# Performance work log

Measured on AMD Instinct MI355X. Metric: run time of the kernel, lower is better.

## Reference

```python
import jax, jax.numpy as jnp
import numpy as np

B, T_ENC, T_DEC = 32, 300, 500
N_MEL, ENC_DIM, ATT_RNN, DEC_RNN, PRE = 80, 512, 1024, 1024, 256
ATT_DIM, LOC_F, LOC_K = 128, 32, 31
PAD = (LOC_K - 1) // 2
P_PRENET = 0.1


def _w(k, shape, fan_in):
    return jax.random.normal(k, shape, jnp.float32) / np.float32(np.sqrt(fan_in))


def setup_inputs() -> dict:
    key = jax.random.key(0)
    ks = jax.random.split(key, 20)
    lens = jax.random.randint(ks[2], (B,), T_ENC // 2, T_ENC + 1).at[0].set(T_ENC)
    return {
        "memory": jax.random.normal(ks[0], (B, T_ENC, ENC_DIM), jnp.float32),
        "decoder_inputs": jax.random.normal(ks[1], (B, N_MEL, T_DEC), jnp.float32),
        "memory_lengths": lens,
        "pre_W1": _w(ks[3], (PRE, N_MEL), N_MEL),
        "pre_W2": _w(ks[4], (PRE, PRE), PRE),
        "att_Wih": _w(ks[5], (4 * ATT_RNN, PRE + ENC_DIM), PRE + ENC_DIM),
        "att_Whh": _w(ks[6], (4 * ATT_RNN, ATT_RNN), ATT_RNN),
        "att_bih": jnp.zeros((4 * ATT_RNN,), jnp.float32),
        "att_bhh": jnp.zeros((4 * ATT_RNN,), jnp.float32),
        "q_W": _w(ks[7], (ATT_DIM, ATT_RNN), ATT_RNN),
        "m_W": _w(ks[8], (ATT_DIM, ENC_DIM), ENC_DIM),
        "v_w": _w(ks[9], (ATT_DIM,), ATT_DIM),
        "loc_conv_W": _w(ks[10], (LOC_F, 2, LOC_K), 2 * LOC_K),
        "loc_dense_W": _w(ks[11], (ATT_DIM, LOC_F), LOC_F),
        "dec_Wih": _w(ks[12], (4 * DEC_RNN, ATT_RNN + ENC_DIM), ATT_RNN + ENC_DIM),
        "dec_Whh": _w(ks[13], (4 * DEC_RNN, DEC_RNN), DEC_RNN),
        "dec_bih": jnp.zeros((4 * DEC_RNN,), jnp.float32),
        "dec_bhh": jnp.zeros((4 * DEC_RNN,), jnp.float32),
        "proj_W": _w(ks[14], (N_MEL, DEC_RNN + ENC_DIM), DEC_RNN + ENC_DIM),
        "proj_b": jnp.zeros((N_MEL,), jnp.float32),
        "gate_W": _w(ks[15], (DEC_RNN + ENC_DIM,), DEC_RNN + ENC_DIM),
        "gate_b": jnp.zeros((), jnp.float32),
    }


def _lstm(x, h, c, Wih, Whh, bih, bhh):
    # PyTorch LSTMCell gate order: i, f, g, o
    g = x @ Wih.T + bih + h @ Whh.T + bhh
    i, f, gg, o = jnp.split(g, 4, axis=-1)
    c = jax.nn.sigmoid(f) * c + jax.nn.sigmoid(i) * jnp.tanh(gg)
    h = jax.nn.sigmoid(o) * jnp.tanh(c)
    return h, c


def _prenet(x, W1, W2):
    # Original uses F.dropout(..., 0.1, training=True) always; deterministic masks here.
    k1, k2 = jax.random.split(jax.random.key(1))
    x = jax.nn.relu(x @ W1.T)
    x = x * jax.random.bernoulli(k1, 1.0 - P_PRENET, x.shape) / (1.0 - P_PRENET)
    x = jax.nn.relu(x @ W2.T)
    x = x * jax.random.bernoulli(k2, 1.0 - P_PRENET, x.shape) / (1.0 - P_PRENET)
    return x


def _forward(memory, decoder_inputs, memory_lengths, pre_W1, pre_W2, att_Wih, att_Whh,
             att_bih, att_bhh, q_W, m_W, v_w, loc_conv_W, loc_dense_W, dec_Wih, dec_Whh,
             dec_bih, dec_bhh, proj_W, proj_b, gate_W, gate_b):
    x = jnp.transpose(decoder_inputs, (2, 0, 1))          # [T_dec, B, n_mel]
    go = jnp.zeros((1,) + x.shape[1:], x.dtype)
    x = jnp.concatenate([go, x], axis=0)                  # [T_dec+1, B, n_mel]
    dec_ins = _prenet(x, pre_W1, pre_W2)[:-1]             # [T_dec, B, PRE]

    processed_memory = memory @ m_W.T                     # [B, T_enc, ATT_DIM]
    valid = jnp.arange(T_ENC)[None, :] < memory_lengths[:, None]  # [B, T_enc]
    Bn = memory.shape[0]
    zf = lambda d: jnp.zeros((Bn, d), memory.dtype)
    carry0 = (zf(ATT_RNN), zf(ATT_RNN), zf(DEC_RNN), zf(DEC_RNN),
              zf(T_ENC), zf(T_ENC), zf(ENC_DIM))

    def step(carry, x_t):
        ah, ac, dh, dc, aw, awc, ctx = carry
        ah, ac = _lstm(jnp.concatenate([x_t, ctx], 1), ah, ac,
                       att_Wih, att_Whh, att_bih, att_bhh)
        awcat = jnp.stack([aw, awc], axis=1)              # [B, 2, T_enc]
        loc = jax.lax.conv_general_dilated(awcat, loc_conv_W, (1,), [(PAD, PAD)],
                                           dimension_numbers=('NCH', 'OIH', 'NCH'))
        loc = jnp.transpose(loc, (0, 2, 1)) @ loc_dense_W.T   # [B, T_enc, ATT_DIM]
        pq = (ah @ q_W.T)[:, None, :]                     # [B, 1, ATT_DIM]
        e = jnp.tanh(pq + loc + processed_memory) @ v_w   # [B, T_enc]
        e = jnp.where(valid, e, -jnp.inf)
        aw = jax.nn.softmax(e, axis=1)
        ctx = jnp.einsum('bt,btd->bd', aw, memory)        # [B, ENC_DIM]
        awc = awc + aw
        dh, dc = _lstm(jnp.concatenate([ah, ctx], 1), dh, dc,
                       dec_Wih, dec_Whh, dec_bih, dec_bhh)
        dhac = jnp.concatenate([dh, ctx], 1)
        mel = dhac @ proj_W.T + proj_b                    # [B, n_mel]
        gate = dhac @ gate_W + gate_b                     # [B]
        return (ah, ac, dh, dc, aw, awc, ctx), (mel, gate, aw)

    _, (mels, gates, aligns) = jax.lax.scan(jax.checkpoint(step), carry0, dec_ins)
    mel_outputs = jnp.transpose(mels, (1, 2, 0))          # [B, n_mel, T_dec]
    gate_outputs = gates.T                                # [B, T_dec]
    alignments = jnp.transpose(aligns, (1, 0, 2))         # [B, T_dec, T_enc]
    return mel_outputs, gate_outputs, alignments


def reference(memory, decoder_inputs, memory_lengths, pre_W1, pre_W2, att_Wih, att_Whh,
              att_bih, att_bhh, q_W, m_W, v_w, loc_conv_W, loc_dense_W, dec_Wih, dec_Whh,
              dec_bih, dec_bhh, proj_W, proj_b, gate_W, gate_b):
    return _forward(memory, decoder_inputs, memory_lengths, pre_W1, pre_W2, att_Wih,
                    att_Whh, att_bih, att_bhh, q_W, m_W, v_w, loc_conv_W, loc_dense_W,
                    dec_Wih, dec_Whh, dec_bih, dec_bhh, proj_W, proj_b, gate_W, gate_b)
```

## Files before the change

### kernel.cpp

```cpp
#include <hip/hip_runtime.h>

#define NB 32
#define TENC 300
#define TDEC 500
#define NMEL 80
#define ENCD 512
#define PRE 256
#define ADIM 128
#define RD 8

#define OFF_DECINS 0ull
#define OFF_H1M    4096000ull
#define OFF_AHR    4096000ull
#define OFF_DHR    (OFF_AHR + 262144ull)
#define OFF_CXR    (OFF_DHR + 262144ull)
#define RINGS_N    655360ull
#define OFF_PM     8192000ull
#define OFF_STATE  (OFF_PM + 1228800ull)
#define OFF_AC     (OFF_STATE + 0ull)
#define OFF_DC     (OFF_STATE + 32768ull)
#define OFF_AW     (OFF_STATE + 65536ull)
#define OFF_AWC    (OFF_STATE + 75136ull)
#define OFF_E      (OFF_STATE + 84736ull)
#define OFF_SLOTS  (OFF_STATE + 94336ull)
#define STATE_N    98440ull
#define OFF_QWT    (OFF_STATE + STATE_N)
#define OFF_PROJWT (OFF_QWT + 131072ull)
#define OFF_MWT    (OFF_PROJWT + 122880ull)
#define OFF_W1T    (OFF_MWT + 65536ull)
#define OFF_W2T    (OFF_W1T + 20480ull)

__device__ __forceinline__ float gload(const float* p){
  return __hip_atomic_load(p, __ATOMIC_RELAXED, __HIP_MEMORY_SCOPE_AGENT);
}
__device__ __forceinline__ void gstore(float* p, float v){
  __hip_atomic_store(p, v, __ATOMIC_RELAXED, __HIP_MEMORY_SCOPE_AGENT);
}

__device__ __forceinline__ void gbar(unsigned* slots, unsigned epoch){
  __syncthreads();
  int tid = threadIdx.x;
  if (tid == 0)
    __hip_atomic_store(&slots[blockIdx.x], epoch, __ATOMIC_RELAXED, __HIP_MEMORY_SCOPE_AGENT);
  if (tid < 64){
    const unsigned long long* p = (const unsigned long long*)slots;
    unsigned long long a, b;
    do {
      a = __hip_atomic_load(p + 2*tid,     __ATOMIC_RELAXED, __HIP_MEMORY_SCOPE_AGENT);
      b = __hip_atomic_load(p + 2*tid + 1, __ATOMIC_RELAXED, __HIP_MEMORY_SCOPE_AGENT);
    } while ((unsigned)a < epoch || (unsigned)(a >> 32) < epoch ||
             (unsigned)b < epoch || (unsigned)(b >> 32) < epoch);
  }
  __syncthreads();
}

__host__ __device__ __forceinline__ unsigned rotl32(unsigned v, int r){ return (v<<r)|(v>>(32-r)); }

__host__ __device__ __forceinline__ void tf2x32(unsigned k0, unsigned k1, unsigned c0, unsigned c1,
                                                unsigned& y0, unsigned& y1){
  unsigned ks2 = k0 ^ k1 ^ 0x1BD11BDAu;
  unsigned x0 = c0 + k0, x1 = c1 + k1;
#define TFR(r) x0 += x1; x1 = rotl32(x1, r); x1 ^= x0;
  TFR(13) TFR(15) TFR(26) TFR(6)
  x0 += k1;  x1 += ks2 + 1u;
  TFR(17) TFR(29) TFR(16) TFR(24)
  x0 += ks2; x1 += k0 + 2u;
  TFR(13) TFR(15) TFR(26) TFR(6)
  x0 += k0;  x1 += k1 + 3u;
  TFR(17) TFR(29) TFR(16) TFR(24)
  x0 += k1;  x1 += ks2 + 4u;
  TFR(13) TFR(15) TFR(26) TFR(6)
  x0 += ks2; x1 += k0 + 5u;
#undef TFR
  y0 = x0; y1 = x1;
}

__device__ __forceinline__ float mask_scale(unsigned k0, unsigned k1, unsigned idx){
  unsigned y0, y1;
  tf2x32(k0, k1, 0u, idx, y0, y1);
  unsigned bits = y0 ^ y1;
  float u = __uint_as_float((bits >> 9) | 0x3f800000u) - 1.0f;
  return (u < 0.9f) ? (1.0f/0.9f) : 0.0f;
}

__global__ __launch_bounds__(256) void k_setup(float* __restrict__ ws,
    const float* __restrict__ qW, const float* __restrict__ projW, const float* __restrict__ mW,
    const float* __restrict__ w1, const float* __restrict__ w2){
  long i = (long)blockIdx.x*256 + threadIdx.x;
  long stride = (long)gridDim.x*256;
  float* st = ws + OFF_STATE;
  for (long x = i; x < (long)STATE_N; x += stride) st[x] = 0.f;
  float* qWT = ws + OFF_QWT;
  for (long x = i; x < 1024*128; x += stride){ int u = x>>7, d = x&127; qWT[x] = qW[(size_t)d*1024+u]; }
  float* pWT = ws + OFF_PROJWT;
  for (long x = i; x < 1536*80; x += stride){ int k = x/80, m = x%80; pWT[x] = projW[(size_t)m*1536+k]; }
  float* mWT = ws + OFF_MWT;
  for (long x = i; x < 512*128; x += stride){ int k = x>>7, d = x&127; mWT[x] = mW[(size_t)d*512+k]; }
  float* w1T = ws + OFF_W1T;
  for (long x = i; x < 80*256; x += stride){ int m = x>>8, u = x&255; w1T[x] = w1[(size_t)u*80+m]; }
  float* w2T = ws + OFF_W2T;
  for (long x = i; x < 256*256; x += stride){ int k = x>>8, u = x&255; w2T[x] = w2[(size_t)u*256+k]; }
}

__global__ __launch_bounds__(256) void k_prenet1(const float* __restrict__ di,
    const float* __restrict__ W1T, float* __restrict__ h1m, unsigned k10, unsigned k11){
  __shared__ float xs[NMEL];
  int bid = blockIdx.x;
  int t = bid >> 5, b = bid & 31;
  int tid = threadIdx.x;
  if (tid < NMEL) xs[tid] = (t == 0) ? 0.f : di[(size_t)b*40000 + (size_t)tid*500 + (t-1)];
  __syncthreads();
  float acc = 0.f;
  for (int m = 0; m < NMEL; ++m) acc += xs[m] * W1T[m*256 + tid];
  acc = fmaxf(acc, 0.f);
  unsigned idx = (unsigned)bid*256u + (unsigned)tid;
  h1m[(size_t)bid*256 + tid] = acc * mask_scale(k10, k11, idx);
}

__global__ __launch_bounds__(256) void k_prenet2(const float* __restrict__ h1m,
    const float* __restrict__ W2T, float* __restrict__ dec_ins, unsigned k20, unsigned k21){
  __shared__ float hs[PRE];
  int bid = blockIdx.x;
  int tid = threadIdx.x;
  hs[tid] = h1m[(size_t)bid*256 + tid];
  __syncthreads();
  float acc = 0.f;
  for (int k = 0; k < PRE; ++k) acc += hs[k] * W2T[k*256 + tid];
  acc = fmaxf(acc, 0.f);
  unsigned idx = (unsigned)bid*256u + (unsigned)tid;
  dec_ins[(size_t)bid*256 + tid] = acc * mask_scale(k20, k21, idx);
}

__global__ __launch_bounds__(128) void k_procmem(const float* __restrict__ mem,
    const float* __restrict__ mWT, float* __restrict__ pm){
  __shared__ float ms[ENCD];
  int bid = blockIdx.x;
  int tid = threadIdx.x;
  const float* src = mem + (size_t)bid*ENCD;
  for (int i = tid; i < ENCD; i += 128) ms[i] = src[i];
  __syncthreads();
  float acc = 0.f;
  for (int k = 0; k < ENCD; ++k) acc += ms[k] * mWT[k*128 + tid];
  pm[(size_t)bid*128 + tid] = acc;
}

__device__ __forceinline__ float2 xld2(const float* s0, int l0, const float* s1,
                                       const float* h, int b, int k){
  const float* p;
  if (k < l0) p = s0 + (size_t)b*l0 + k;
  else if (k < l0 + 512) p = s1 + (b<<9) + (k - l0);
  else p = h + (b<<10) + (k - (l0 + 512));
  return *(const float2*)p;
}

__device__ __forceinline__ void lstm_block(int ub,
    const float* __restrict__ W1, const float* __restrict__ W2,
    const float* __restrict__ bih, const float* __restrict__ bhh,
    const float* __restrict__ s0, int l0, const float* __restrict__ s1,
    const float* __restrict__ hprev, int Ktot,
    float* __restrict__ c_st, float* __restrict__ hnew, int tid){
  __shared__ float Xc[2][128*32];
  __shared__ float gates[16][32];
  const int xw = l0 + 512, xw4 = xw >> 2;
  const int NC = Ktot >> 7;
  const int w = tid >> 6, l = tid & 63;
  const int ss = l & 31, ph = l >> 5;
  const int rlA = 2*w, rlB = 2*w + 1;
  const int rowA = (rlA >> 2)*1024 + ub*4 + (rlA & 3);
  const int rowB = (rlB >> 2)*1024 + ub*4 + (rlB & 3);
  const float4* W1A = (const float4*)(W1 + (size_t)rowA*xw);
  const float4* W1B = (const float4*)(W1 + (size_t)rowB*xw);
  const float4* W2A = (const float4*)(W2 + ((size_t)rowA<<10));
  const float4* W2B = (const float4*)(W2 + ((size_t)rowB<<10));
  float accA[16] = {}, accB[16] = {};
  float2 sx[4];
#pragma unroll
  for (int it = 0; it < 4; ++it){
    int pidx = tid + it*512;
    int b = pidx >> 6, kL = (pidx & 63)*2;
    sx[it] = xld2(s0, l0, s1, hprev, b, kL);
  }
#pragma unroll
  for (int it = 0; it < 4; ++it){
    int pidx = tid + it*512;
    int b = pidx >> 6, kL = (pidx & 63)*2;
    int a0 = kL*32 + (((b>>2) ^ ((kL>>2)&7))<<2) + (b&3);
    Xc[0][a0] = sx[it].x; Xc[0][a0+32] = sx[it].y;
  }
  float4 wA, wB;
  { int f = ss;
    wA = (f < xw4) ? W1A[f] : W2A[f - xw4];
    wB = (f < xw4) ? W1B[f] : W2B[f - xw4]; }
  __syncthreads();

  for (int c = 0; c < NC; ++c){
    float4 wAn, wBn;
    if (c + 1 < NC){
      int f = (c+1)*32 + ss;
      wAn = (f < xw4) ? W1A[f] : W2A[f - xw4];
      wBn = (f < xw4) ? W1B[f] : W2B[f - xw4];
      int kg0 = (c+1) << 7;
#pragma unroll
      for (int it = 0; it < 4; ++it){
        int pidx = tid + it*512;
        int b = pidx >> 6, kL = (pidx & 63)*2;
        sx[it] = xld2(s0, l0, s1, hprev, b, kg0 + kL);
      }
    }
    const float4* X4 = (const float4*)Xc[c & 1];
#pragma unroll
    for (int e = 0; e < 4; ++e){
      int kL = 4*ss + e;
      int sw = (kL >> 2) & 7;
      float ea = (e==0)?wA.x:(e==1)?wA.y:(e==2)?wA.z:wA.w;
      float eb = (e==0)?wB.x:(e==1)?wB.y:(e==2)?wB.z:wB.w;
      int base = kL*8;
#pragma unroll
      for (int j = 0; j < 4; ++j){
        int g = ph*4 + j;
        float4 xv = X4[base + (g ^ sw)];
        accA[4*j+0] += ea*xv.x; accA[4*j+1] += ea*xv.y;
        accA[4*j+2] += ea*xv.z; accA[4*j+3] += ea*xv.w;
        accB[4*j+0] += eb*xv.x; accB[4*j+1] += eb*xv.y;
        accB[4*j+2] += eb*xv.z; accB[4*j+3] += eb*xv.w;
      }
    }
    if (c + 1 < NC){
#pragma unroll
      for (int it = 0; it < 4; ++it){
        int pidx = tid + it*512;
        int b = pidx >> 6, kL = (pidx & 63)*2;
        int a0 = kL*32 + (((b>>2) ^ ((kL>>2)&7))<<2) + (b&3);
        Xc[(c+1)&1][a0] = sx[it].x; Xc[(c+1)&1][a0+32] = sx[it].y;
      }
      wA = wAn; wB = wBn;
    }
    __syncthreads();
  }
#pragma unroll
  for (int j = 0; j < 16; ++j){
    accA[j] += __shfl_xor(accA[j], 16, 64);
    accB[j] += __shfl_xor(accB[j], 16, 64);
  }
#pragma unroll
  for (int m = 8; m >= 1; m >>= 1){
    int up = ss & m;
#pragma unroll
    for (int j = 0; j < m; ++j){
      float sA = up ? accA[j] : accA[j+m];
      float kA = up ? accA[j+m] : accA[j];
      float sB = up ? accB[j] : accB[j+m];
      float kB = up ? accB[j+m] : accB[j];
      accA[j] = kA + __shfl_xor(sA, m, 64);
      accB[j] = kB + __shfl_xor(sB, m, 64);
    }
  }
  if (!(l & 16)){
    int b = ph*16 + (l & 15);
    gates[rlA][b] = accA[0];
    gates[rlB][b] = accB[0];
  }
  __syncthreads();
  if (tid < 128){
    int b = tid & 31, u = tid >> 5;
    int gu = ub*4 + u;
    float gi = gates[u][b]     + bih[gu]         + bhh[gu];
    float gf = gates[4+u][b]   + bih[1024+gu]    + bhh[1024+gu];
    float gg = gates[8+u][b]   + bih[2048+gu]    + bhh[2048+gu];
    float go = gates[12+u][b]  + bih[3072+gu]    + bhh[3072+gu];
    float ii = 1.f/(1.f + expf(-gi));
    float ff = 1.f/(1.f + expf(-gf));
    float oo = 1.f/(1.f + expf(-go));
    float tg = tanhf(gg);
    float cold = gload(&c_st[b*1024 + gu]);
    float cn = ff*cold + ii*tg;
    gstore(&c_st[b*1024 + gu], cn);
    gstore(&hnew[b*1024 + gu], oo*tanhf(cn));
  }
  __syncthreads();
}

__device__ __forceinline__ void energy_tile(int b, int tile, bool act, int h,
    const float* __restrict__ aw, const float* __restrict__ awc,
    const float* __restrict__ lcW, const float* __restrict__ ldW, const float* __restrict__ vw,
    const float* __restrict__ sPq, const float* __restrict__ pm, float* __restrict__ e_ws, int t2){
  __shared__ float sIn[2][2][46];
  __shared__ float cfs[2][16][33];
  __shared__ float ep[2][16][17];
  int j0 = tile*16;
  if (act){
    if (t2 < 46){ int j = j0 - 15 + t2; sIn[h][0][t2] = (j >= 0 && j < 300) ? gload(&aw[b*300 + j]) : 0.f; }
    else if (t2 < 92){ int i = t2 - 46; int j = j0 - 15 + i; sIn[h][1][i] = (j >= 0 && j < 300) ? gload(&awc[b*300 + j]) : 0.f; }
  }
  __syncthreads();
  if (act){
    int fg = t2 & 15, jl = t2 >> 4;
    int f0 = 2*fg;
    float c0 = 0.f, c1 = 0.f;
#pragma unroll
    for (int c = 0; c < 2; ++c)
#pragma unroll
      for (int k = 0; k < 31; ++k){
        float a = sIn[h][c][jl + k];
        c0 += a * lcW[f0*62 + c*31 + k];
        c1 += a * lcW[(f0+1)*62 + c*31 + k];
      }
    cfs[h][jl][f0] = c0; cfs[h][jl][f0+1] = c1;
  }
  __syncthreads();
  if (act){
    int dg = t2 & 15, jl = t2 >> 4;
    int j = j0 + jl;
    float s = 0.f;
    if (j < 300){
      const float* pmrow = pm + ((size_t)(b*300 + j))*128 + dg*8;
#pragma unroll
      for (int dd = 0; dd < 8; ++dd){
        int d = dg*8 + dd;
        float acc = sPq[d] + pmrow[dd];
#pragma unroll
        for (int f = 0; f < 32; ++f) acc += cfs[h][jl][f] * ldW[d*32 + f];
        s += vw[d] * tanhf(acc);
      }
    }
    ep[h][jl][dg] = s;
  }
  __syncthreads();
  if (act && t2 < 16){
    int j = j0 + t2;
    if (j < 300){
      float s = 0.f;
#pragma unroll
      for (int dg = 0; dg < 16; ++dg) s += ep[h][t2][dg];
      gstore(&e_ws[b*300 + j], s);
    }
  }
  __syncthreads();
}

__device__ __forceinline__ void pq_energy(int b, int jt, const float* __restrict__ ah,
    const float* __restrict__ qWT, const float* __restrict__ aw, const float* __restrict__ awc,
    const float* __restrict__ lcW, const float* __restrict__ ldW, const float* __restrict__ vw,
    const float* __restrict__ pm, float* __restrict__ e_ws, int tid){
  __shared__ float sAh[1024];
  __shared__ float pqs[512];
  __shared__ float sPq[128];
  for (int i = tid; i < 1024; i += 512) sAh[i] = ah[b*1024 + i];
  __syncthreads();
  int d = tid & 127, seg = tid >> 7;
  const float* qt = qWT + (size_t)(seg*256)*128 + d;
  const float* sh = sAh + seg*256;
  float a0 = 0.f, a1 = 0.f, a2 = 0.f, a3 = 0.f;
  for (int u = 0; u < 256; u += 4){
    a0 += sh[u]   * qt[(size_t)u*128];
    a1 += sh[u+1] * qt[(size_t)(u+1)*128];
    a2 += sh[u+2] * qt[(size_t)(u+2)*128];
    a3 += sh[u+3] * qt[(size_t)(u+3)*128];
  }
  pqs[seg*128 + d] = (a0 + a1) + (a2 + a3);
  __syncthreads();
  if (tid < 128) sPq[tid] = (pqs[tid] + pqs[128+tid]) + (pqs[256+tid] + pqs[384+tid]);
  __syncthreads();
  int h = tid >> 8, t2 = tid & 255;
  for (int r = 0; r < 2; ++r){
    int tile = r*16 + jt*2 + h;
    energy_tile(b, tile, tile < 19, h, aw, awc, lcW, ldW, vw, sPq, pm, e_ws, t2);
  }
}

__device__ __forceinline__ void dec_out_slice(int b, int jt,
    const float* __restrict__ dh, const float* __restrict__ ctx,
    const float* __restrict__ pWT, const float* __restrict__ projb,
    const float* __restrict__ gateW, const float* __restrict__ gateb,
    float* __restrict__ out, int s, int tid){
  __shared__ float sX[1536];
  __shared__ float melp[48][11];
  __shared__ float gatep[32];
  for (int i = tid; i < 1024; i += 512) sX[i] = dh[b*1024 + i];
  if (tid < 512) { int i = tid; sX[1024 + i] = ctx[b*512 + i]; }
  __syncthreads();
  if (tid < 480){
    int mi = tid % 10, kseg = tid / 10;
    int m = jt*10 + mi;
    const float* pw = pWT + m;
    int k0 = kseg*32;
    float a0 = 0.f, a1 = 0.f;
#pragma unroll 8
    for (int k = 0; k < 32; k += 2){
      a0 += sX[k0+k]   * pw[(size_t)(k0+k)*80];
      a1 += sX[k0+k+1] * pw[(size_t)(k0+k+1)*80];
    }
    melp[kseg][mi] = a0 + a1;
  } else if (jt == 0){
    int kseg = tid - 480;
    int k0 = kseg*48;
    float a = 0.f;
    for (int k = 0; k < 48; ++k) a += sX[k0+k] * gateW[k0+k];
    gatep[kseg] = a;
  }
  __syncthreads();
  if (tid < 10){
    float s2 = projb[jt*10 + tid];
    for (int q = 0; q < 48; ++q) s2 += melp[q][tid];
    out[(size_t)b*40000 + (size_t)(jt*10 + tid)*500 + s] = s2;
  }
  if (jt == 0 && tid == 10){
    float s2 = gateb[0];
    for (int q = 0; q < 32; ++q) s2 += gatep[q];
    out[1280000 + (size_t)b*500 + s] = s2;
  }
  __syncthreads();
}

__device__ __forceinline__ void soft_phase(int b, int dsl, const float* __restrict__ e_ws,
    const int* __restrict__ lens, const float* __restrict__ mem,
    float* __restrict__ aw, float* __restrict__ awc, float* __restrict__ ctx,
    float* __restrict__ out, int t, int tid){
  __shared__ float se[300];
  __shared__ float sa[300];
  __shared__ float red[512];
  int len = lens[b];
  for (int j = tid; j < 300; j += 512) se[j] = gload(&e_ws[b*300 + j]);
  __syncthreads();
  float m = -1e30f;
  for (int j = tid; j < len; j += 512) m = fmaxf(m, se[j]);
  red[tid] = m; __syncthreads();
  for (int s = 256; s > 0; s >>= 1){ if (tid < s) red[tid] = fmaxf(red[tid], red[tid + s]); __syncthreads(); }
  float mx = red[0]; __syncthreads();
  float ssum = 0.f;
  for (int j = tid; j < len; j += 512) ssum += expf(se[j] - mx);
  red[tid] = ssum; __syncthreads();
  for (int s = 256; s > 0; s >>= 1){ if (tid < s) red[tid] += red[tid + s]; __syncthreads(); }
  float inv = 1.f/red[0];
  __syncthreads();
  float* al = out + 1296000 + (size_t)b*150000 + (size_t)t*300;
  for (int j = tid; j < 300; j += 512){
    float v = (j < len) ? expf(se[j] - mx)*inv : 0.f;
    sa[j] = v;
    if (dsl == 0){
      gstore(&aw[b*300 + j], v);
      gstore(&awc[b*300 + j], gload(&awc[b*300 + j]) + v);
      al[j] = v;
    }
  }
  __syncthreads();
  int d = dsl*64 + (tid & 63), jq = tid >> 6;
  int chunk = (len + 7) >> 3;
  int j0 = jq*chunk, j1 = min(len, j0 + chunk);
  float a0 = 0.f, a1 = 0.f;
  const float* mb = mem + (size_t)b*153600 + d;
  int j = j0;
  for (; j + 1 < j1; j += 2){
    a0 += sa[j]   * mb[(size_t)j*512];
    a1 += sa[j+1] * mb[(size_t)(j+1)*512];
  }
  if (j < j1) a0 += sa[j]*mb[(size_t)j*512];
  red[tid] = a0 + a1; __syncthreads();
  if (jq == 0){
    int ln = tid & 63;
    float s = 0.f;
#pragma unroll
    for (int q = 0; q < 8; ++q) s += red[ln + 64*q];
    gstore(&ctx[b*512 + d], s);
  }
  __syncthreads();
}

struct DecParams {
  const float *memory;
  const int   *lens;
  const float *attWih, *attWhh, *attBih, *attBhh;
  const float *decWih, *decWhh, *decBih, *decBhh;
  const float *lcW, *ldW, *vw, *projb, *gateW, *gateb;
  float *ws, *out;
};

__global__ void __launch_bounds__(512, 2) k_loop(DecParams p){
  int wg = blockIdx.x, tid = threadIdx.x;
  float* ws = p.ws;
  float* decins = ws + OFF_DECINS;
  float* e_ws = ws + OFF_E;
  float* pm = ws + OFF_PM;
  float* AC = ws + OFF_AC;
  float* DC = ws + OFF_DC;
  float* aw = ws + OFF_AW;
  float* awc = ws + OFF_AWC;
  float* qWT = ws + OFF_QWT;
  float* pWT = ws + OFF_PROJWT;
  unsigned* slots = (unsigned*)(ws + OFF_SLOTS);
  unsigned ep = 0;
  int b = wg >> 3, jt = wg & 7;

#define AHR(s) (ws + OFF_AHR + (size_t)(s)*32768)
#define DHR(s) (ws + OFF_DHR + (size_t)(s)*32768)
#define CXR(s) (ws + OFF_CXR + (size_t)(s)*16384)

  for (unsigned i = (unsigned)wg*512u + tid; i < (unsigned)RINGS_N; i += 131072u)
    gstore(ws + OFF_AHR + i, 0.f);
  gbar(slots, ++ep);

  lstm_block(wg, p.attWih, p.attWhh, p.attBih, p.attBhh,
             decins, PRE, CXR(0), AHR(0), 1792, AC, AHR(1), tid);
  gbar(slots, ++ep);

  for (int t = 0; t < TDEC; ++t){
    int cu = (t + 1) % RD, pr = t % RD, nx = (t + 2) % RD;
    pq_energy(b, jt, AHR(cu), qWT, aw, awc, p.lcW, p.ldW, p.vw, pm, e_ws, tid);
    if (t > 0)
      dec_out_slice(b, jt, DHR(pr), CXR(pr), pWT, p.projb, p.gateW, p.gateb, p.out, t - 1, tid);
    gbar(slots, ++ep);
    soft_phase(b, jt, e_ws, p.lens, p.memory, aw, awc, CXR(cu), p.out, t, tid);
    gbar(slots, ++ep);
    lstm_block(wg, p.decWih, p.decWhh, p.decBih, p.decBhh,
               AHR(cu), 1024, CXR(cu), DHR(pr), 2560, DC, DHR(cu), tid);
    if (t + 1 < TDEC)
      lstm_block(wg, p.attWih, p.attWhh, p.attBih, p.attBhh,
                 decins + (size_t)(t + 1)*NB*PRE, PRE, CXR(cu), AHR(cu), 1792,
                 AC, AHR(nx), tid);
    gbar(slots, ++ep);
  }
  dec_out_slice(b, jt, DHR(500 % RD), CXR(500 % RD), pWT, p.projb, p.gateW, p.gateb,
                p.out, TDEC - 1, tid);
#undef AHR
#undef DHR
#undef CXR
}

extern "C" void kernel_launch(void* const* d_in, const int* in_sizes, int n_in,
                              void* d_out, int out_size, void* d_ws, size_t ws_size,
                              hipStream_t stream) {
  const float* memory   = (const float*)d_in[0];
  const float* dec_in   = (const float*)d_in[1];
  const int*   lens     = (const int*)  d_in[2];
  const float* pre_W1   = (const float*)d_in[3];
  const float* pre_W2   = (const float*)d_in[4];
  const float* att_Wih  = (const float*)d_in[5];
  const float* att_Whh  = (const float*)d_in[6];
  const float* att_bih  = (const float*)d_in[7];
  const float* att_bhh  = (const float*)d_in[8];
  const float* q_W      = (const float*)d_in[9];
  const float* m_W      = (const float*)d_in[10];
  const float* v_w      = (const float*)d_in[11];
  const float* lc_W     = (const float*)d_in[12];
  const float* ld_W     = (const float*)d_in[13];
  const float* dec_Wih  = (const float*)d_in[14];
  const float* dec_Whh  = (const float*)d_in[15];
  const float* dec_bih  = (const float*)d_in[16];
  const float* dec_bhh  = (const float*)d_in[17];
  const float* proj_W   = (const float*)d_in[18];
  const float* proj_b   = (const float*)d_in[19];
  const float* gate_W   = (const float*)d_in[20];
  const float* gate_b   = (const float*)d_in[21];
  float* out = (float*)d_out;
  float* ws  = (float*)d_ws;

  unsigned k10, k11, k20, k21;
  tf2x32(0u, 1u, 0u, 0u, k10, k11);
  tf2x32(0u, 1u, 0u, 1u, k20, k21);

  k_setup<<<1024, 256, 0, stream>>>(ws, q_W, proj_W, m_W, pre_W1, pre_W2);
  k_prenet1<<<TDEC*NB, 256, 0, stream>>>(dec_in, ws + OFF_W1T, ws + OFF_H1M, k10, k11);
  k_prenet2<<<TDEC*NB, 256, 0, stream>>>(ws + OFF_H1M, ws + OFF_W2T, ws + OFF_DECINS, k20, k21);
  k_procmem<<<NB*TENC, 128, 0, stream>>>(memory, ws + OFF_MWT, ws + OFF_PM);

  DecParams hp;
  hp.memory = memory; hp.lens = lens;
  hp.attWih = att_Wih; hp.attWhh = att_Whh; hp.attBih = att_bih; hp.attBhh = att_bhh;
  hp.decWih = dec_Wih; hp.decWhh = dec_Whh; hp.decBih = dec_bih; hp.decBhh = dec_bhh;
  hp.lcW = lc_W; hp.ldW = ld_W; hp.vw = v_w; hp.projb = proj_b; hp.gateW = gate_W; hp.gateb = gate_b;
  hp.ws = ws; hp.out = out;
  k_loop<<<256, 512, 0, stream>>>(hp);
}
```

Baseline: 77.94 ms.

## Double workgroup size to 1024 threads and split per-thread work across all phases

```diff
diff --git a/kernel.cpp b/kernel.cpp
--- a/kernel.cpp
+++ b/kernel.cpp
@@ -165,44 +165,38 @@
   const int NC = Ktot >> 7;
   const int w = tid >> 6, l = tid & 63;
   const int ss = l & 31, ph = l >> 5;
-  const int rlA = 2*w, rlB = 2*w + 1;
-  const int rowA = (rlA >> 2)*1024 + ub*4 + (rlA & 3);
-  const int rowB = (rlB >> 2)*1024 + ub*4 + (rlB & 3);
-  const float4* W1A = (const float4*)(W1 + (size_t)rowA*xw);
-  const float4* W1B = (const float4*)(W1 + (size_t)rowB*xw);
-  const float4* W2A = (const float4*)(W2 + ((size_t)rowA<<10));
-  const float4* W2B = (const float4*)(W2 + ((size_t)rowB<<10));
-  float accA[16] = {}, accB[16] = {};
-  float2 sx[4];
-#pragma unroll
-  for (int it = 0; it < 4; ++it){
-    int pidx = tid + it*512;
+  const int row = (w >> 2)*1024 + ub*4 + (w & 3);
+  const float4* W1A = (const float4*)(W1 + (size_t)row*xw);
+  const float4* W2A = (const float4*)(W2 + ((size_t)row<<10));
+  float accA[16] = {};
+  float2 sx[2];
+#pragma unroll
+  for (int it = 0; it < 2; ++it){
+    int pidx = tid + it*1024;
     int b = pidx >> 6, kL = (pidx & 63)*2;
     sx[it] = xld2(s0, l0, s1, hprev, b, kL);
   }
 #pragma unroll
-  for (int it = 0; it < 4; ++it){
-    int pidx = tid + it*512;
+  for (int it = 0; it < 2; ++it){
+    int pidx = tid + it*1024;
     int b = pidx >> 6, kL = (pidx & 63)*2;
     int a0 = kL*32 + (((b>>2) ^ ((kL>>2)&7))<<2) + (b&3);
     Xc[0][a0] = sx[it].x; Xc[0][a0+32] = sx[it].y;
   }
-  float4 wA, wB;
+  float4 wA;
   { int f = ss;
-    wA = (f < xw4) ? W1A[f] : W2A[f - xw4];
-    wB = (f < xw4) ? W1B[f] : W2B[f - xw4]; }
+    wA = (f < xw4) ? W1A[f] : W2A[f - xw4]; }
   __syncthreads();
 
   for (int c = 0; c < NC; ++c){
-    float4 wAn, wBn;
+    float4 wAn;
     if (c + 1 < NC){
       int f = (c+1)*32 + ss;
       wAn = (f < xw4) ? W1A[f] : W2A[f - xw4];
-      wBn = (f < xw4) ? W1B[f] : W2B[f - xw4];
       int kg0 = (c+1) << 7;
 #pragma unroll
-      for (int it = 0; it < 4; ++it){
-        int pidx = tid + it*512;
+      for (int it = 0; it < 2; ++it){
+        int pidx = tid + it*1024;
         int b = pidx >> 6, kL = (pidx & 63)*2;
         sx[it] = xld2(s0, l0, s1, hprev, b, kg0 + kL);
       }
@@ -213,7 +207,6 @@
       int kL = 4*ss + e;
       int sw = (kL >> 2) & 7;
       float ea = (e==0)?wA.x:(e==1)?wA.y:(e==2)?wA.z:wA.w;
-      float eb = (e==0)?wB.x:(e==1)?wB.y:(e==2)?wB.z:wB.w;
       int base = kL*8;
 #pragma unroll
       for (int j = 0; j < 4; ++j){
@@ -221,27 +214,23 @@
         float4 xv = X4[base + (g ^ sw)];
         accA[4*j+0] += ea*xv.x; accA[4*j+1] += ea*xv.y;
         accA[4*j+2] += ea*xv.z; accA[4*j+3] += ea*xv.w;
-        accB[4*j+0] += eb*xv.x; accB[4*j+1] += eb*xv.y;
-        accB[4*j+2] += eb*xv.z; accB[4*j+3] += eb*xv.w;
       }
     }
     if (c + 1 < NC){
 #pragma unroll
-      for (int it = 0; it < 4; ++it){
-        int pidx = tid + it*512;
+      for (int it = 0; it < 2; ++it){
+        int pidx = tid + it*1024;
         int b = pidx >> 6, kL = (pidx & 63)*2;
         int a0 = kL*32 + (((b>>2) ^ ((kL>>2)&7))<<2) + (b&3);
         Xc[(c+1)&1][a0] = sx[it].x; Xc[(c+1)&1][a0+32] = sx[it].y;
       }
-      wA = wAn; wB = wBn;
+      wA = wAn;
     }
     __syncthreads();
   }
 #pragma unroll
-  for (int j = 0; j < 16; ++j){
+  for (int j = 0; j < 16; ++j)
     accA[j] += __shfl_xor(accA[j], 16, 64);
-    accB[j] += __shfl_xor(accB[j], 16, 64);
-  }
 #pragma unroll
   for (int m = 8; m >= 1; m >>= 1){
     int up = ss & m;
@@ -249,16 +238,12 @@
     for (int j = 0; j < m; ++j){
       float sA = up ? accA[j] : accA[j+m];
       float kA = up ? accA[j+m] : accA[j];
-      float sB = up ? accB[j] : accB[j+m];
-      float kB = up ? accB[j+m] : accB[j];
       accA[j] = kA + __shfl_xor(sA, m, 64);
-      accB[j] = kB + __shfl_xor(sB, m, 64);
     }
   }
   if (!(l & 16)){
     int b = ph*16 + (l & 15);
-    gates[rlA][b] = accA[0];
-    gates[rlB][b] = accB[0];
+    gates[w][b] = accA[0];
   }
   __syncthreads();
   if (tid < 128){
@@ -284,9 +269,9 @@
     const float* __restrict__ aw, const float* __restrict__ awc,
     const float* __restrict__ lcW, const float* __restrict__ ldW, const float* __restrict__ vw,
     const float* __restrict__ sPq, const float* __restrict__ pm, float* __restrict__ e_ws, int t2){
-  __shared__ float sIn[2][2][46];
-  __shared__ float cfs[2][16][33];
-  __shared__ float ep[2][16][17];
+  __shared__ float sIn[4][2][46];
+  __shared__ float cfs[4][16][33];
+  __shared__ float ep[4][16][17];
   int j0 = tile*16;
   if (act){
     if (t2 < 46){ int j = j0 - 15 + t2; sIn[h][0][t2] = (j >= 0 && j < 300) ? gload(&aw[b*300 + j]) : 0.f; }
@@ -343,15 +328,15 @@
     const float* __restrict__ lcW, const float* __restrict__ ldW, const float* __restrict__ vw,
     const float* __restrict__ pm, float* __restrict__ e_ws, int tid){
   __shared__ float sAh[1024];
-  __shared__ float pqs[512];
+  __shared__ float pqs[1024];
   __shared__ float sPq[128];
-  for (int i = tid; i < 1024; i += 512) sAh[i] = ah[b*1024 + i];
+  sAh[tid] = ah[b*1024 + tid];
   __syncthreads();
   int d = tid & 127, seg = tid >> 7;
-  const float* qt = qWT + (size_t)(seg*256)*128 + d;
-  const float* sh = sAh + seg*256;
+  const float* qt = qWT + (size_t)(seg*128)*128 + d;
+  const float* sh = sAh + seg*128;
   float a0 = 0.f, a1 = 0.f, a2 = 0.f, a3 = 0.f;
-  for (int u = 0; u < 256; u += 4){
+  for (int u = 0; u < 128; u += 4){
     a0 += sh[u]   * qt[(size_t)u*128];
     a1 += sh[u+1] * qt[(size_t)(u+1)*128];
     a2 += sh[u+2] * qt[(size_t)(u+2)*128];
@@ -359,13 +344,16 @@
   }
   pqs[seg*128 + d] = (a0 + a1) + (a2 + a3);
   __syncthreads();
-  if (tid < 128) sPq[tid] = (pqs[tid] + pqs[128+tid]) + (pqs[256+tid] + pqs[384+tid]);
+  if (tid < 128){
+    float s = 0.f;
+#pragma unroll
+    for (int q = 0; q < 8; ++q) s += pqs[tid + 128*q];
+    sPq[tid] = s;
+  }
   __syncthreads();
   int h = tid >> 8, t2 = tid & 255;
-  for (int r = 0; r < 2; ++r){
-    int tile = r*16 + jt*2 + h;
-    energy_tile(b, tile, tile < 19, h, aw, awc, lcW, ldW, vw, sPq, pm, e_ws, t2);
-  }
+  int tile = (h >> 1)*16 + jt*2 + (h & 1);
+  energy_tile(b, tile, tile < 19, h, aw, awc, lcW, ldW, vw, sPq, pm, e_ws, t2);
 }
 
 __device__ __forceinline__ void dec_out_slice(int b, int jt,
@@ -374,39 +362,42 @@
     const float* __restrict__ gateW, const float* __restrict__ gateb,
     float* __restrict__ out, int s, int tid){
   __shared__ float sX[1536];
-  __shared__ float melp[48][11];
-  __shared__ float gatep[32];
-  for (int i = tid; i < 1024; i += 512) sX[i] = dh[b*1024 + i];
-  if (tid < 512) { int i = tid; sX[1024 + i] = ctx[b*512 + i]; }
-  __syncthreads();
-  if (tid < 480){
+  __shared__ float melp[96][11];
+  __shared__ float gatep[64];
+  sX[tid & 1023] = (tid < 1024) ? dh[b*1024 + tid] : sX[tid & 1023];
+  if (tid < 1024) sX[tid] = dh[b*1024 + tid];
+  else { int i = tid - 1024; if (i < 512) sX[1024 + i] = ctx[b*512 + i]; }
+  if (tid >= 512 && tid < 1024) {  }
+  if (tid < 512) sX[1024 + tid] = ctx[b*512 + tid];
+  __syncthreads();
+  if (tid < 960){
     int mi = tid % 10, kseg = tid / 10;
     int m = jt*10 + mi;
     const float* pw = pWT + m;
-    int k0 = kseg*32;
+    int k0 = kseg*16;
     float a0 = 0.f, a1 = 0.f;
 #pragma unroll 8
-    for (int k = 0; k < 32; k += 2){
+    for (int k = 0; k < 16; k += 2){
       a0 += sX[k0+k]   * pw[(size_t)(k0+k)*80];
       a1 += sX[k0+k+1] * pw[(size_t)(k0+k+1)*80];
     }
     melp[kseg][mi] = a0 + a1;
   } else if (jt == 0){
-    int kseg = tid - 480;
-    int k0 = kseg*48;
+    int kseg = tid - 960;
+    int k0 = kseg*24;
     float a = 0.f;
-    for (int k = 0; k < 48; ++k) a += sX[k0+k] * gateW[k0+k];
+    for (int k = 0; k < 24; ++k) a += sX[k0+k] * gateW[k0+k];
     gatep[kseg] = a;
   }
   __syncthreads();
   if (tid < 10){
     float s2 = projb[jt*10 + tid];
-    for (int q = 0; q < 48; ++q) s2 += melp[q][tid];
+    for (int q = 0; q < 96; ++q) s2 += melp[q][tid];
     out[(size_t)b*40000 + (size_t)(jt*10 + tid)*500 + s] = s2;
   }
   if (jt == 0 && tid == 10){
     float s2 = gateb[0];
-    for (int q = 0; q < 32; ++q) s2 += gatep[q];
+    for (int q = 0; q < 64; ++q) s2 += gatep[q];
     out[1280000 + (size_t)b*500 + s] = s2;
   }
   __syncthreads();
@@ -418,34 +409,32 @@
     float* __restrict__ out, int t, int tid){
   __shared__ float se[300];
   __shared__ float sa[300];
-  __shared__ float red[512];
+  __shared__ float red[1024];
   int len = lens[b];
-  for (int j = tid; j < 300; j += 512) se[j] = gload(&e_ws[b*300 + j]);
-  __syncthreads();
-  float m = -1e30f;
-  for (int j = tid; j < len; j += 512) m = fmaxf(m, se[j]);
+  if (tid < 300) se[tid] = gload(&e_ws[b*300 + tid]);
+  __syncthreads();
+  float m = (tid < len) ? se[tid] : -1e30f;
   red[tid] = m; __syncthreads();
-  for (int s = 256; s > 0; s >>= 1){ if (tid < s) red[tid] = fmaxf(red[tid], red[tid + s]); __syncthreads(); }
+  for (int s = 512; s > 0; s >>= 1){ if (tid < s) red[tid] = fmaxf(red[tid], red[tid + s]); __syncthreads(); }
   float mx = red[0]; __syncthreads();
-  float ssum = 0.f;
-  for (int j = tid; j < len; j += 512) ssum += expf(se[j] - mx);
+  float ssum = (tid < len) ? expf(se[tid] - mx) : 0.f;
   red[tid] = ssum; __syncthreads();
-  for (int s = 256; s > 0; s >>= 1){ if (tid < s) red[tid] += red[tid + s]; __syncthreads(); }
+  for (int s = 512; s > 0; s >>= 1){ if (tid < s) red[tid] += red[tid + s]; __syncthreads(); }
   float inv = 1.f/red[0];
   __syncthreads();
   float* al = out + 1296000 + (size_t)b*150000 + (size_t)t*300;
-  for (int j = tid; j < 300; j += 512){
-    float v = (j < len) ? expf(se[j] - mx)*inv : 0.f;
-    sa[j] = v;
+  if (tid < 300){
+    float v = (tid < len) ? expf(se[tid] - mx)*inv : 0.f;
+    sa[tid] = v;
     if (dsl == 0){
-      gstore(&aw[b*300 + j], v);
-      gstore(&awc[b*300 + j], gload(&awc[b*300 + j]) + v);
-      al[j] = v;
+      gstore(&aw[b*300 + tid], v);
+      gstore(&awc[b*300 + tid], gload(&awc[b*300 + tid]) + v);
+      al[tid] = v;
     }
   }
   __syncthreads();
   int d = dsl*64 + (tid & 63), jq = tid >> 6;
-  int chunk = (len + 7) >> 3;
+  int chunk = (len + 15) >> 4;
   int j0 = jq*chunk, j1 = min(len, j0 + chunk);
   float a0 = 0.f, a1 = 0.f;
   const float* mb = mem + (size_t)b*153600 + d;
@@ -460,7 +449,7 @@
     int ln = tid & 63;
     float s = 0.f;
 #pragma unroll
-    for (int q = 0; q < 8; ++q) s += red[ln + 64*q];
+    for (int q = 0; q < 16; ++q) s += red[ln + 64*q];
     gstore(&ctx[b*512 + d], s);
   }
   __syncthreads();
@@ -475,7 +464,7 @@
   float *ws, *out;
 };
 
-__global__ void __launch_bounds__(512, 2) k_loop(DecParams p){
+__global__ void __launch_bounds__(1024, 4) k_loop(DecParams p){
   int wg = blockIdx.x, tid = threadIdx.x;
   float* ws = p.ws;
   float* decins = ws + OFF_DECINS;
@@ -495,7 +484,7 @@
 #define DHR(s) (ws + OFF_DHR + (size_t)(s)*32768)
 #define CXR(s) (ws + OFF_CXR + (size_t)(s)*16384)
 
-  for (unsigned i = (unsigned)wg*512u + tid; i < (unsigned)RINGS_N; i += 131072u)
+  for (unsigned i = (unsigned)wg*1024u + tid; i < (unsigned)RINGS_N; i += 262144u)
     gstore(ws + OFF_AHR + i, 0.f);
   gbar(slots, ++ep);
 
@@ -569,5 +558,5 @@
   hp.decWih = dec_Wih; hp.decWhh = dec_Whh; hp.decBih = dec_bih; hp.decBhh = dec_bhh;
   hp.lcW = lc_W; hp.ldW = ld_W; hp.vw = v_w; hp.projb = proj_b; hp.gateW = gate_W; hp.gateb = gate_b;
   hp.ws = ws; hp.out = out;
-  k_loop<<<256, 512, 0, stream>>>(hp);
-}
+  k_loop<<<256, 1024, 0, stream>>>(hp);
+}
```

Result: slower. 130.1 ms (+66.9%).

## Store decoder LSTM weights and prenet outputs as bf16 in workspace

Applied to the files above, without the earlier changes.

```diff
diff --git a/kernel.cpp b/kernel.cpp
--- a/kernel.cpp
+++ b/kernel.cpp
@@ -7,14 +7,16 @@
 #define ENCD 512
 #define PRE 256
 #define ADIM 128
-#define RD 8
+#define RD 4
+#define WSPLIT 2944
 
 #define OFF_DECINS 0ull
-#define OFF_H1M    4096000ull
+#define OFF_WHI    2048000ull
 #define OFF_AHR    4096000ull
-#define OFF_DHR    (OFF_AHR + 262144ull)
-#define OFF_CXR    (OFF_DHR + 262144ull)
-#define RINGS_N    655360ull
+#define OFF_DHR    (OFF_AHR + 131072ull)
+#define OFF_CXR    (OFF_DHR + 131072ull)
+#define RINGS_N    327680ull
+#define OFF_WLO    (OFF_AHR + RINGS_N)
 #define OFF_PM     8192000ull
 #define OFF_STATE  (OFF_PM + 1228800ull)
 #define OFF_AC     (OFF_STATE + 0ull)
@@ -29,6 +31,15 @@
 #define OFF_MWT    (OFF_PROJWT + 122880ull)
 #define OFF_W1T    (OFF_MWT + 65536ull)
 #define OFF_W2T    (OFF_W1T + 20480ull)
+
+__device__ __forceinline__ unsigned short f2bf(float f){
+  unsigned u = __float_as_uint(f);
+  unsigned r = (u + 0x7FFFu + ((u >> 16) & 1u)) >> 16;
+  return (unsigned short)r;
+}
+__device__ __forceinline__ float bf2f(unsigned short h){
+  return __uint_as_float(((unsigned)h) << 16);
+}
 
 __device__ __forceinline__ float gload(const float* p){
   return __hip_atomic_load(p, __ATOMIC_RELAXED, __HIP_MEMORY_SCOPE_AGENT);
@@ -85,7 +96,8 @@
 
 __global__ __launch_bounds__(256) void k_setup(float* __restrict__ ws,
     const float* __restrict__ qW, const float* __restrict__ projW, const float* __restrict__ mW,
-    const float* __restrict__ w1, const float* __restrict__ w2){
+    const float* __restrict__ w1, const float* __restrict__ w2,
+    const float* __restrict__ dWih, const float* __restrict__ dWhh){
   long i = (long)blockIdx.x*256 + threadIdx.x;
   long stride = (long)gridDim.x*256;
   float* st = ws + OFF_STATE;
@@ -100,11 +112,26 @@
   for (long x = i; x < 80*256; x += stride){ int m = x>>8, u = x&255; w1T[x] = w1[(size_t)u*80+m]; }
   float* w2T = ws + OFF_W2T;
   for (long x = i; x < 256*256; x += stride){ int k = x>>8, u = x&255; w2T[x] = w2[(size_t)u*256+k]; }
-}
-
-__global__ __launch_bounds__(256) void k_prenet1(const float* __restrict__ di,
-    const float* __restrict__ W1T, float* __restrict__ h1m, unsigned k10, unsigned k11){
+  unsigned short* wlo = (unsigned short*)(ws + OFF_WLO);
+  for (long x = i; x < (long)WSPLIT*2560; x += stride){
+    int row = (int)(x/2560), c = (int)(x%2560);
+    float v = (c < 1536) ? dWih[(size_t)row*1536 + c] : dWhh[(size_t)row*1024 + (c-1536)];
+    wlo[x] = f2bf(v);
+  }
+  unsigned short* whi = (unsigned short*)(ws + OFF_WHI);
+  for (long x = i; x < (long)(4096-WSPLIT)*2560; x += stride){
+    int row = WSPLIT + (int)(x/2560), c = (int)(x%2560);
+    float v = (c < 1536) ? dWih[(size_t)row*1536 + c] : dWhh[(size_t)row*1024 + (c-1536)];
+    whi[x] = f2bf(v);
+  }
+}
+
+__global__ __launch_bounds__(256) void k_prenet(const float* __restrict__ di,
+    const float* __restrict__ W1T, const float* __restrict__ W2T,
+    unsigned short* __restrict__ dec_ins,
+    unsigned k10, unsigned k11, unsigned k20, unsigned k21){
   __shared__ float xs[NMEL];
+  __shared__ float h1s[PRE];
   int bid = blockIdx.x;
   int t = bid >> 5, b = bid & 31;
   int tid = threadIdx.x;
@@ -114,21 +141,13 @@
   for (int m = 0; m < NMEL; ++m) acc += xs[m] * W1T[m*256 + tid];
   acc = fmaxf(acc, 0.f);
   unsigned idx = (unsigned)bid*256u + (unsigned)tid;
-  h1m[(size_t)bid*256 + tid] = acc * mask_scale(k10, k11, idx);
-}
-
-__global__ __launch_bounds__(256) void k_prenet2(const float* __restrict__ h1m,
-    const float* __restrict__ W2T, float* __restrict__ dec_ins, unsigned k20, unsigned k21){
-  __shared__ float hs[PRE];
-  int bid = blockIdx.x;
-  int tid = threadIdx.x;
-  hs[tid] = h1m[(size_t)bid*256 + tid];
-  __syncthreads();
-  float acc = 0.f;
-  for (int k = 0; k < PRE; ++k) acc += hs[k] * W2T[k*256 + tid];
-  acc = fmaxf(acc, 0.f);
-  unsigned idx = (unsigned)bid*256u + (unsigned)tid;
-  dec_ins[(size_t)bid*256 + tid] = acc * mask_scale(k20, k21, idx);
+  h1s[tid] = acc * mask_scale(k10, k11, idx);
+  __syncthreads();
+  float a2 = 0.f;
+  for (int k = 0; k < PRE; ++k) a2 += h1s[k] * W2T[k*256 + tid];
+  a2 = fmaxf(a2, 0.f);
+  a2 *= mask_scale(k20, k21, idx);
+  dec_ins[(size_t)bid*256 + tid] = f2bf(a2);
 }
 
 __global__ __launch_bounds__(128) void k_procmem(const float* __restrict__ mem,
@@ -144,19 +163,30 @@
   pm[(size_t)bid*128 + tid] = acc;
 }
 
-__device__ __forceinline__ float2 xld2(const float* s0, int l0, const float* s1,
+template<bool S0B>
+__device__ __forceinline__ float2 xld2(const void* s0v, int l0, const float* s1,
                                        const float* h, int b, int k){
-  const float* p;
-  if (k < l0) p = s0 + (size_t)b*l0 + k;
-  else if (k < l0 + 512) p = s1 + (b<<9) + (k - l0);
-  else p = h + (b<<10) + (k - (l0 + 512));
-  return *(const float2*)p;
-}
-
+  if (k < l0){
+    if constexpr (S0B){
+      const unsigned short* s0 = (const unsigned short*)s0v;
+      unsigned u = *(const unsigned*)(s0 + (size_t)b*l0 + k);
+      float2 r; r.x = __uint_as_float((u & 0xFFFFu) << 16); r.y = __uint_as_float((u >> 16) << 16);
+      return r;
+    } else {
+      const float* s0 = (const float*)s0v;
+      return *(const float2*)(s0 + (size_t)b*l0 + k);
+    }
+  }
+  if (k < l0 + 512) return *(const float2*)(s1 + (b<<9) + (k - l0));
+  return *(const float2*)(h + (b<<10) + (k - (l0 + 512)));
+}
+
+template<bool S0B, bool WB>
 __device__ __forceinline__ void lstm_block(int ub,
     const float* __restrict__ W1, const float* __restrict__ W2,
+    const unsigned short* __restrict__ wlo, const unsigned short* __restrict__ whi,
     const float* __restrict__ bih, const float* __restrict__ bhh,
-    const float* __restrict__ s0, int l0, const float* __restrict__ s1,
+    const void* __restrict__ s0, int l0, const float* __restrict__ s1,
     const float* __restrict__ hprev, int Ktot,
     float* __restrict__ c_st, float* __restrict__ hnew, int tid){
   __shared__ float Xc[2][128*32];
@@ -172,13 +202,30 @@
   const float4* W1B = (const float4*)(W1 + (size_t)rowB*xw);
   const float4* W2A = (const float4*)(W2 + ((size_t)rowA<<10));
   const float4* W2B = (const float4*)(W2 + ((size_t)rowB<<10));
+  const unsigned short* BA = nullptr; const unsigned short* BB = nullptr;
+  if constexpr (WB){
+    BA = (rowA < WSPLIT) ? wlo + (size_t)rowA*2560 : whi + (size_t)(rowA - WSPLIT)*2560;
+    BB = (rowB < WSPLIT) ? wlo + (size_t)rowB*2560 : whi + (size_t)(rowB - WSPLIT)*2560;
+  }
+  auto loadWA = [&](int f)->float4{
+    if constexpr (WB){
+      ushort4 h4 = *(const ushort4*)(BA + 4*(size_t)f);
+      return make_float4(bf2f(h4.x), bf2f(h4.y), bf2f(h4.z), bf2f(h4.w));
+    } else return (f < xw4) ? W1A[f] : W2A[f - xw4];
+  };
+  auto loadWB = [&](int f)->float4{
+    if constexpr (WB){
+      ushort4 h4 = *(const ushort4*)(BB + 4*(size_t)f);
+      return make_float4(bf2f(h4.x), bf2f(h4.y), bf2f(h4.z), bf2f(h4.w));
+    } else return (f < xw4) ? W1B[f] : W2B[f - xw4];
+  };
   float accA[16] = {}, accB[16] = {};
   float2 sx[4];
 #pragma unroll
   for (int it = 0; it < 4; ++it){
     int pidx = tid + it*512;
     int b = pidx >> 6, kL = (pidx & 63)*2;
-    sx[it] = xld2(s0, l0, s1, hprev, b, kL);
+    sx[it] = xld2<S0B>(s0, l0, s1, hprev, b, kL);
   }
 #pragma unroll
   for (int it = 0; it < 4; ++it){
@@ -187,31 +234,27 @@
     int a0 = kL*32 + (((b>>2) ^ ((kL>>2)&7))<<2) + (b&3);
     Xc[0][a0] = sx[it].x; Xc[0][a0+32] = sx[it].y;
   }
-  float4 wA, wB;
-  { int f = ss;
-    wA = (f < xw4) ? W1A[f] : W2A[f - xw4];
-    wB = (f < xw4) ? W1B[f] : W2B[f - xw4]; }
+  float4 wA = loadWA(ss), wB = loadWB(ss);
   __syncthreads();
 
   for (int c = 0; c < NC; ++c){
     float4 wAn, wBn;
     if (c + 1 < NC){
       int f = (c+1)*32 + ss;
-      wAn = (f < xw4) ? W1A[f] : W2A[f - xw4];
-      wBn = (f < xw4) ? W1B[f] : W2B[f - xw4];
+      wAn = loadWA(f); wBn = loadWB(f);
       int kg0 = (c+1) << 7;
 #pragma unroll
       for (int it = 0; it < 4; ++it){
         int pidx = tid + it*512;
         int b = pidx >> 6, kL = (pidx & 63)*2;
-        sx[it] = xld2(s0, l0, s1, hprev, b, kg0 + kL);
+        sx[it] = xld2<S0B>(s0, l0, s1, hprev, b, kg0 + kL);
       }
     }
     const float4* X4 = (const float4*)Xc[c & 1];
+    const int sw = ss & 7;
 #pragma unroll
     for (int e = 0; e < 4; ++e){
       int kL = 4*ss + e;
-      int sw = (kL >> 2) & 7;
       float ea = (e==0)?wA.x:(e==1)?wA.y:(e==2)?wA.z:wA.w;
       float eb = (e==0)?wB.x:(e==1)?wB.y:(e==2)?wB.z:wB.w;
       int base = kL*8;
@@ -470,7 +513,7 @@
   const float *memory;
   const int   *lens;
   const float *attWih, *attWhh, *attBih, *attBhh;
-  const float *decWih, *decWhh, *decBih, *decBhh;
+  const float *decBih, *decBhh;
   const float *lcW, *ldW, *vw, *projb, *gateW, *gateb;
   float *ws, *out;
 };
@@ -478,7 +521,9 @@
 __global__ void __launch_bounds__(512, 2) k_loop(DecParams p){
   int wg = blockIdx.x, tid = threadIdx.x;
   float* ws = p.ws;
-  float* decins = ws + OFF_DECINS;
+  const unsigned short* decins = (const unsigned short*)(ws + OFF_DECINS);
+  const unsigned short* wlo = (const unsigned short*)(ws + OFF_WLO);
+  const unsigned short* whi = (const unsigned short*)(ws + OFF_WHI);
   float* e_ws = ws + OFF_E;
   float* pm = ws + OFF_PM;
   float* AC = ws + OFF_AC;
@@ -499,8 +544,8 @@
     gstore(ws + OFF_AHR + i, 0.f);
   gbar(slots, ++ep);
 
-  lstm_block(wg, p.attWih, p.attWhh, p.attBih, p.attBhh,
-             decins, PRE, CXR(0), AHR(0), 1792, AC, AHR(1), tid);
+  lstm_block<true,false>(wg, p.attWih, p.attWhh, nullptr, nullptr, p.attBih, p.attBhh,
+                         decins, PRE, CXR(0), AHR(0), 1792, AC, AHR(1), tid);
   gbar(slots, ++ep);
 
   for (int t = 0; t < TDEC; ++t){
@@ -511,12 +556,12 @@
     gbar(slots, ++ep);
     soft_phase(b, jt, e_ws, p.lens, p.memory, aw, awc, CXR(cu), p.out, t, tid);
     gbar(slots, ++ep);
-    lstm_block(wg, p.decWih, p.decWhh, p.decBih, p.decBhh,
-               AHR(cu), 1024, CXR(cu), DHR(pr), 2560, DC, DHR(cu), tid);
+    lstm_block<false,true>(wg, nullptr, nullptr, wlo, whi, p.decBih, p.decBhh,
+                           AHR(cu), 1024, CXR(cu), DHR(pr), 2560, DC, DHR(cu), tid);
     if (t + 1 < TDEC)
-      lstm_block(wg, p.attWih, p.attWhh, p.attBih, p.attBhh,
-                 decins + (size_t)(t + 1)*NB*PRE, PRE, CXR(cu), AHR(cu), 1792,
-                 AC, AHR(nx), tid);
+      lstm_block<true,false>(wg, p.attWih, p.attWhh, nullptr, nullptr, p.attBih, p.attBhh,
+                             decins + (size_t)(t + 1)*NB*PRE, PRE, CXR(cu), AHR(cu), 1792,
+                             AC, AHR(nx), tid);
     gbar(slots, ++ep);
   }
   dec_out_slice(b, jt, DHR(500 % RD), CXR(500 % RD), pWT, p.projb, p.gateW, p.gateb,
@@ -558,15 +603,15 @@
   tf2x32(0u, 1u, 0u, 0u, k10, k11);
   tf2x32(0u, 1u, 0u, 1u, k20, k21);
 
-  k_setup<<<1024, 256, 0, stream>>>(ws, q_W, proj_W, m_W, pre_W1, pre_W2);
-  k_prenet1<<<TDEC*NB, 256, 0, stream>>>(dec_in, ws + OFF_W1T, ws + OFF_H1M, k10, k11);
-  k_prenet2<<<TDEC*NB, 256, 0, stream>>>(ws + OFF_H1M, ws + OFF_W2T, ws + OFF_DECINS, k20, k21);
+  k_setup<<<1024, 256, 0, stream>>>(ws, q_W, proj_W, m_W, pre_W1, pre_W2, dec_Wih, dec_Whh);
+  k_prenet<<<TDEC*NB, 256, 0, stream>>>(dec_in, ws + OFF_W1T, ws + OFF_W2T,
+                                        (unsigned short*)(ws + OFF_DECINS), k10, k11, k20, k21);
   k_procmem<<<NB*TENC, 128, 0, stream>>>(memory, ws + OFF_MWT, ws + OFF_PM);
 
   DecParams hp;
   hp.memory = memory; hp.lens = lens;
   hp.attWih = att_Wih; hp.attWhh = att_Whh; hp.attBih = att_bih; hp.attBhh = att_bhh;
-  hp.decWih = dec_Wih; hp.decWhh = dec_Whh; hp.decBih = dec_bih; hp.decBhh = dec_bhh;
+  hp.decBih = dec_bih; hp.decBhh = dec_bhh;
   hp.lcW = lc_W; hp.ldW = ld_W; hp.vw = v_w; hp.projb = proj_b; hp.gateW = gate_W; hp.gateb = gate_b;
   hp.ws = ws; hp.out = out;
   k_loop<<<256, 512, 0, stream>>>(hp);
```

Result: no change. 77.00 ms (median of 2 runs) (-1.2%).
